# Optimization experiments

Hardware: AMD Instinct MI355X
Metric: run time of the kernel (lower is better)

## Reference

```python
import jax, jax.numpy as jnp
import numpy as np

EPS = 1e-5
H, W, C, NCLS = 8, 16, 64, 8

def _bn_params(key, c):
    k1, k2, k3, k4 = jax.random.split(key, 4)
    gamma = jax.random.uniform(k1, (c,), minval=0.5, maxval=1.5)
    beta = 0.1 * jax.random.normal(k2, (c,))
    mean = 0.1 * jax.random.normal(k3, (c,))
    var = jax.random.uniform(k4, (c,), minval=0.5, maxval=1.5)
    return jnp.stack([gamma, beta, mean, var]).astype(jnp.float32)  # (4, c)

def bn2d(x, p):
    # eval-mode BatchNorm2d; p: (4, C); x: (B, C, H, W)
    g, b, m, v = p[0], p[1], p[2], p[3]
    s = g * jax.lax.rsqrt(v + EPS)
    return x * s[None, :, None, None] + (b - m * s)[None, :, None, None]

def bn1d_scalar(x, p):
    # eval-mode BatchNorm1d with 1 channel; p: (4, 1); x: (B, 1, F)
    g, b, m, v = p[0], p[1], p[2], p[3]
    s = g * jax.lax.rsqrt(v + EPS)
    return x * s + (b - m * s)

def conv_same(x, w, b):
    y = jax.lax.conv_general_dilated(x, w, (1, 1), 'SAME',
                                     dimension_numbers=('NCHW', 'OIHW', 'NCHW'))
    return y + b[None, :, None, None]

def setup_inputs() -> dict:
    key = jax.random.key(0)
    ks = jax.random.split(key, 24)
    B = 8192
    d = {}
    d['x'] = jax.random.normal(ks[0], (B, 1, H, W), dtype=jnp.float32)
    d['bn0'] = _bn_params(ks[1], 1)
    d['conv1_w'] = 0.1 * jax.random.normal(ks[2], (C, 1, 3, 3), dtype=jnp.float32)
    d['conv1_b'] = jnp.zeros((C,), jnp.float32)
    d['bn1'] = _bn_params(ks[3], C)
    d['conv2_w'] = (0.1 / np.sqrt(C)) * jax.random.normal(ks[4], (C, C, 3, 3), dtype=jnp.float32)
    d['conv2_b'] = jnp.zeros((C,), jnp.float32)
    d['bn2'] = _bn_params(ks[5], C)
    # LocallyConnected2d, kernel_size=1 -> per-pixel (out_c, in_c) weights
    d['lc3_w'] = (1.0 / np.sqrt(C)) * jax.random.normal(ks[6], (C, C, H, W), dtype=jnp.float32)
    d['bn3'] = _bn_params(ks[7], C)
    d['lc4_w'] = (1.0 / np.sqrt(C)) * jax.random.normal(ks[8], (C, C, H, W), dtype=jnp.float32)
    d['bn4'] = _bn_params(ks[9], C)
    F5 = H * W * C
    d['fc5_w'] = (1.0 / np.sqrt(F5)) * jax.random.normal(ks[10], (512, F5), dtype=jnp.float32)
    d['fc5_b'] = jnp.zeros((512,), jnp.float32)
    d['bn5'] = _bn_params(ks[11], 1)
    d['fc6_w'] = (1.0 / np.sqrt(512)) * jax.random.normal(ks[12], (512, 512), dtype=jnp.float32)
    d['fc6_b'] = jnp.zeros((512,), jnp.float32)
    d['bn6'] = _bn_params(ks[13], 1)
    d['fc7_w'] = (1.0 / np.sqrt(512)) * jax.random.normal(ks[14], (128, 512), dtype=jnp.float32)
    d['fc7_b'] = jnp.zeros((128,), jnp.float32)
    d['bn7'] = _bn_params(ks[15], 1)
    d['fc8_w'] = (1.0 / np.sqrt(128)) * jax.random.normal(ks[16], (NCLS, 128), dtype=jnp.float32)
    d['fc8_b'] = jnp.zeros((NCLS,), jnp.float32)
    return d

def reference(x, bn0, conv1_w, conv1_b, bn1, conv2_w, conv2_b, bn2,
              lc3_w, bn3, lc4_w, bn4, fc5_w, fc5_b, bn5,
              fc6_w, fc6_b, bn6, fc7_w, fc7_b, bn7, fc8_w, fc8_b):
    B = x.shape[0]
    # squeeze -> view(B, 16, 8) -> transpose(1,2) -> add channel dim
    h = jnp.swapaxes(x.reshape(B, W, H), 1, 2)[:, None]  # (B,1,H,W)
    h = bn2d(h, bn0)
    h = jax.nn.relu(bn2d(conv_same(h, conv1_w, conv1_b), bn1))
    h = jax.nn.relu(bn2d(conv_same(h, conv2_w, conv2_b), bn2))
    # locally connected, k=1: per-pixel channel mixing
    h = jax.nn.relu(bn2d(jnp.einsum('bchw,ochw->bohw', h, lc3_w), bn3))
    h = jax.nn.relu(bn2d(jnp.einsum('bchw,ochw->bohw', h, lc4_w), bn4))
    h = h.reshape(B, 1, -1)  # (B, 1, C*H*W)
    h = h @ fc5_w.T + fc5_b
    h = jax.nn.relu(bn1d_scalar(h, bn5))
    h = jax.nn.relu(bn1d_scalar(h @ fc6_w.T + fc6_b, bn6))
    h = jax.nn.relu(bn1d_scalar(h @ fc7_w.T + fc7_b, bn7))
    h = h @ fc8_w.T + fc8_b
    return h.reshape(B, NCLS)
```

## Files before the change

### kernel.cpp

```cpp
#include <hip/hip_runtime.h>

typedef unsigned short bf16_t;
typedef __attribute__((ext_vector_type(8))) short bf16x8;
typedef __attribute__((ext_vector_type(8))) unsigned short u16x8;
typedef __attribute__((ext_vector_type(4))) float f32x4;

#if defined(__has_builtin)
#if __has_builtin(__builtin_amdgcn_global_load_lds)
#define HAS_GLL 1
#endif
#endif

__device__ __forceinline__ float b2f(bf16_t u) {
    return __uint_as_float(((unsigned int)u) << 16);
}
__device__ __forceinline__ bf16_t f2b(float f) {
    unsigned int x = __float_as_uint(f);
    unsigned int r = x + 0x7fffu + ((x >> 16) & 1u);
    return (bf16_t)(r >> 16);
}
__device__ __forceinline__ float ldf(const void* p, int i, int isf) {
    return isf ? ((const float*)p)[i] : b2f(((const bf16_t*)p)[i]);
}

__device__ __forceinline__ void stg16(const bf16_t* g, bf16_t* l) {
#ifdef HAS_GLL
    __builtin_amdgcn_global_load_lds(
        (const __attribute__((address_space(1))) unsigned int*)g,
        (__attribute__((address_space(3))) unsigned int*)l,
        16, 0, 0);
#else
    *(uint4*)l = *(const uint4*)g;
#endif
}

#define OFF_S0T0 0
#define OFF_W1   16
#define OFF_S1   592
#define OFF_H1   656
#define OFF_S2   720
#define OFF_H2   784
#define OFF_S3   848
#define OFF_H3   912
#define OFF_S4   976
#define OFF_H4   1040
#define OFF_SC5  1104
#define OFF_H5   1112
#define OFF_SC6  1624
#define OFF_H6   1632
#define OFF_SC7  2144
#define OFF_H7   2152
#define OFF_W8   2280
#define OFF_B8   3304
#define OFF_FLAG 4032

__global__ void detect_kernel(const void* xraw, float* prm)
{
    if (threadIdx.x == 0 && blockIdx.x == 0) {
        const unsigned int* w = (const unsigned int*)xraw;
        int good = 0;
        for (int i = 0; i < 64; i++) {
            float f = __uint_as_float(w[i] << 16);
            float a = fabsf(f);
            if (a >= 0.0009765625f && a <= 16.0f) good++;
        }
        prm[OFF_FLAG] = (good >= 32) ? 0.0f : 1.0f;
    }
}

__global__ __launch_bounds__(256) void cvtb_kernel(
    const void* __restrict__ src, bf16_t* __restrict__ dst, int n,
    const float* __restrict__ prm)
{
    const int isf = prm[OFF_FLAG] > 0.5f;
    int i = blockIdx.x * 256 + threadIdx.x;
    if (i < n) dst[i] = isf ? f2b(((const float*)src)[i]) : ((const bf16_t*)src)[i];
}

__global__ __launch_bounds__(256) void pw2_kernel(
    const void* __restrict__ src, bf16_t* __restrict__ dst,
    const float* __restrict__ prm)
{
    const int isf = prm[OFF_FLAG] > 0.5f;
    int i = blockIdx.x * 256 + threadIdx.x;
    if (i >= 36864) return;
    int oc = i / 576, r = i - oc * 576;
    int tap = r >> 6, ic = r & 63;
    dst[i] = f2b(ldf(src, oc * 576 + ic * 9 + tap, isf));
}

__global__ __launch_bounds__(256) void pw34_kernel(
    const void* __restrict__ src, bf16_t* __restrict__ dst,
    const float* __restrict__ prm)
{
    const int isf = prm[OFF_FLAG] > 0.5f;
    int i = blockIdx.x * 256 + threadIdx.x;
    if (i >= 524288) return;
    int p = i >> 12, r = i & 4095;
    int oc = r >> 6, ic = r & 63;
    dst[i] = f2b(ldf(src, oc * 8192 + ic * 128 + p, isf));
}

__global__ __launch_bounds__(256) void pw5_kernel(
    const void* __restrict__ src, bf16_t* __restrict__ dst,
    const float* __restrict__ prm)
{
    const int isf = prm[OFF_FLAG] > 0.5f;
    int i = blockIdx.x * 256 + threadIdx.x;
    if (i >= 4194304) return;
    int nr = i >> 13, r = i & 8191;
    int p = r >> 6, c = r & 63;
    dst[i] = f2b(ldf(src, nr * 8192 + c * 128 + p, isf));
}

__global__ __launch_bounds__(256) void fold_params_kernel(
    const void* bn0p, const void* w1, const void* b1, const void* bn1p,
    const void* b2c, const void* bn2p, const void* bn3p, const void* bn4p,
    const void* b5, const void* bn5p, const void* b6, const void* bn6p,
    const void* b7, const void* bn7p, const void* w8, const void* b8,
    float* prm)
{
    const int isf = prm[OFF_FLAG] > 0.5f;
    const int t = threadIdx.x;

    if (t == 0) {
        float g = ldf(bn0p, 0, isf), be = ldf(bn0p, 1, isf);
        float m = ldf(bn0p, 2, isf), v = ldf(bn0p, 3, isf);
        float s = g * rsqrtf(v + 1e-5f);
        prm[OFF_S0T0] = s; prm[OFF_S0T0 + 1] = be - m * s;
    }
    for (int i = t; i < 576; i += 256) prm[OFF_W1 + i] = ldf(w1, i, isf);

    if (t < 64) {
        {
            float g = ldf(bn1p, t, isf), be = ldf(bn1p, 64 + t, isf);
            float m = ldf(bn1p, 128 + t, isf), v = ldf(bn1p, 192 + t, isf);
            float s = g * rsqrtf(v + 1e-5f);
            prm[OFF_S1 + t] = s;
            prm[OFF_H1 + t] = s * ldf(b1, t, isf) + (be - m * s);
        }
        {
            float g = ldf(bn2p, t, isf), be = ldf(bn2p, 64 + t, isf);
            float m = ldf(bn2p, 128 + t, isf), v = ldf(bn2p, 192 + t, isf);
            float s = g * rsqrtf(v + 1e-5f);
            prm[OFF_S2 + t] = s;
            prm[OFF_H2 + t] = s * ldf(b2c, t, isf) + (be - m * s);
        }
        {
            float g = ldf(bn3p, t, isf), be = ldf(bn3p, 64 + t, isf);
            float m = ldf(bn3p, 128 + t, isf), v = ldf(bn3p, 192 + t, isf);
            float s = g * rsqrtf(v + 1e-5f);
            prm[OFF_S3 + t] = s;
            prm[OFF_H3 + t] = be - m * s;
        }
        {
            float g = ldf(bn4p, t, isf), be = ldf(bn4p, 64 + t, isf);
            float m = ldf(bn4p, 128 + t, isf), v = ldf(bn4p, 192 + t, isf);
            float s = g * rsqrtf(v + 1e-5f);
            prm[OFF_S4 + t] = s;
            prm[OFF_H4 + t] = be - m * s;
        }
    }
    {
        float g = ldf(bn5p, 0, isf), be = ldf(bn5p, 1, isf);
        float m = ldf(bn5p, 2, isf), v = ldf(bn5p, 3, isf);
        float s = g * rsqrtf(v + 1e-5f);
        if (t == 0) prm[OFF_SC5] = s;
        for (int i = t; i < 512; i += 256)
            prm[OFF_H5 + i] = s * ldf(b5, i, isf) + (be - m * s);
    }
    {
        float g = ldf(bn6p, 0, isf), be = ldf(bn6p, 1, isf);
        float m = ldf(bn6p, 2, isf), v = ldf(bn6p, 3, isf);
        float s = g * rsqrtf(v + 1e-5f);
        if (t == 0) prm[OFF_SC6] = s;
        for (int i = t; i < 512; i += 256)
            prm[OFF_H6 + i] = s * ldf(b6, i, isf) + (be - m * s);
    }
    {
        float g = ldf(bn7p, 0, isf), be = ldf(bn7p, 1, isf);
        float m = ldf(bn7p, 2, isf), v = ldf(bn7p, 3, isf);
        float s = g * rsqrtf(v + 1e-5f);
        if (t == 0) prm[OFF_SC7] = s;
        if (t < 128) prm[OFF_H7 + t] = s * ldf(b7, t, isf) + (be - m * s);
    }
    for (int i = t; i < 1024; i += 256) prm[OFF_W8 + i] = ldf(w8, i, isf);
    if (t < 8) prm[OFF_B8 + t] = ldf(b8, t, isf);
}

__global__ __launch_bounds__(256) void conv1_kernel(
    const void* __restrict__ x, const float* __restrict__ prm,
    bf16_t* __restrict__ c1, int Bc, int c0)
{
    __shared__ float xn[180];
    __shared__ float w1s[576];

    const int t = threadIdx.x;
    const int b0 = blockIdx.x * 4;
    const int isf = prm[OFF_FLAG] > 0.5f;
    const float s0 = prm[OFF_S0T0], t0 = prm[OFF_S0T0 + 1];

    for (int i = t; i < 576; i += 256) w1s[i] = prm[OFF_W1 + i];

    const int pg  = t & 31;
    const int oc0 = (t >> 5) * 8;

    float s1[8], h1[8];
    #pragma unroll
    for (int j = 0; j < 8; j++) {
        s1[j] = prm[OFF_S1 + oc0 + j];
        h1[j] = prm[OFF_H1 + oc0 + j];
    }

    for (int s = 0; s < 4; s++) {
        const int b = b0 + s;
        __syncthreads();
        if (t < 180) {
            int row = t / 18, col = t - row * 18;
            float v = 0.f;
            if (row >= 1 && row <= 8 && col >= 1 && col <= 16)
                v = s0 * ldf(x, (c0 + b) * 128 + (col - 1) * 8 + (row - 1), isf) + t0;
            xn[t] = v;
        }
        __syncthreads();

        #pragma unroll
        for (int m = 0; m < 4; m++) {
            int p = pg + 32 * m;
            int h = p >> 4, w = p & 15;
            float r[9];
            #pragma unroll
            for (int dh = 0; dh < 3; dh++)
                #pragma unroll
                for (int dw = 0; dw < 3; dw++)
                    r[dh * 3 + dw] = xn[(h + dh) * 18 + (w + dw)];
            u16x8 o;
            #pragma unroll
            for (int j = 0; j < 8; j++) {
                float acc = 0.f;
                #pragma unroll
                for (int k = 0; k < 9; k++) acc += r[k] * w1s[(oc0 + j) * 9 + k];
                o[j] = f2b(fmaxf(s1[j] * acc + h1[j], 0.f));
            }
            *(u16x8*)(c1 + (size_t)p * Bc * 64 + (size_t)b * 64 + oc0) = o;
        }
    }
}

__global__ __launch_bounds__(256) void fused_mfma_kernel(
    const bf16_t* __restrict__ c1, const bf16_t* __restrict__ w2p,
    const bf16_t* __restrict__ w3p, const bf16_t* __restrict__ w4p,
    const float* __restrict__ prm, bf16_t* __restrict__ bufA, int Bc)
{
    __shared__ bf16_t sm[20480];
    const int t    = threadIdx.x;
    const int lane = t & 63;
    const int wv   = t >> 6;
    const int m0   = blockIdx.x * 256;
    const int p    = blockIdx.y;
    const int h    = p >> 4, w = p & 15;

    const int fr = lane & 15;
    const int fg = lane >> 4;
    const int swz4 = (fr >> 1) & 3;
    const int orow = fg * 4;
    const int ocol = fr;

    const int rA = t >> 2;
    const int gS = (t & 3) ^ ((t >> 3) & 3);

    f32x4 acc[4][4];
    #pragma unroll
    for (int i = 0; i < 4; i++)
        #pragma unroll
        for (int j = 0; j < 4; j++)
            acc[i][j] = (f32x4){0.f, 0.f, 0.f, 0.f};

    {
        if (h > 0 && w > 0) {
            const bf16_t* ab = c1 + (size_t)((h - 1) * 16 + (w - 1)) * Bc * 64
                             + (size_t)m0 * 64;
            #pragma unroll
            for (int u = 0; u < 4; u++) {
                const int c = t + 256 * u;
                const int row = c >> 2;
                const int g = (c & 3) ^ ((c >> 3) & 3);
                stg16(ab + row * 64 + g * 8, sm + c * 8);
            }
            stg16(w2p + rA * 576 + gS * 8, sm + 16384 + t * 8);
        }
    }
    for (int s = 0; s < 18; s++) {
        const int cur = s & 1;
        __syncthreads();
        if (s + 1 < 18) {
            const int s1 = s + 1;
            const int tap = s1 >> 1;
            const int dh = tap / 3 - 1, dw = tap % 3 - 1;
            const int hh = h + dh, ww = w + dw;
            if (hh >= 0 && hh < 8 && ww >= 0 && ww < 16) {
                const int nb = cur ^ 1;
                const int ic0 = (s1 & 1) * 32;
                const bf16_t* ab = c1 + (size_t)(hh * 16 + ww) * Bc * 64
                                 + (size_t)m0 * 64 + ic0;
                #pragma unroll
                for (int u = 0; u < 4; u++) {
                    const int c = t + 256 * u;
                    const int row = c >> 2;
                    const int g = (c & 3) ^ ((c >> 3) & 3);
                    stg16(ab + row * 64 + g * 8, sm + nb * 8192 + c * 8);
                }
                stg16(w2p + rA * 576 + tap * 64 + ic0 + gS * 8,
                      sm + 16384 + nb * 2048 + t * 8);
            }
        }
        {
            const int tap = s >> 1;
            const int dh = tap / 3 - 1, dw = tap % 3 - 1;
            const int hh = h + dh, ww = w + dw;
            if (hh >= 0 && hh < 8 && ww >= 0 && ww < 16) {
                const bf16_t* Ab = sm + cur * 8192;
                const bf16_t* Bb = sm + 16384 + cur * 2048;
                bf16x8 af[4], bf[4];
                #pragma unroll
                for (int i = 0; i < 4; i++)
                    af[i] = *(const bf16x8*)(Ab + ((wv * 64 + i * 16 + fr) * 4 + (fg ^ swz4)) * 8);
                #pragma unroll
                for (int j = 0; j < 4; j++)
                    bf[j] = *(const bf16x8*)(Bb + ((j * 16 + fr) * 4 + (fg ^ swz4)) * 8);
                #pragma unroll
                for (int i = 0; i < 4; i++)
                    #pragma unroll
                    for (int j = 0; j < 4; j++)
                        acc[i][j] = __builtin_amdgcn_mfma_f32_16x16x32_bf16(
                            af[i], bf[j], acc[i][j], 0, 0, 0);
            }
        }
    }
    __syncthreads();

    #pragma unroll
    for (int j = 0; j < 4; j++) {
        const int oc = j * 16 + ocol;
        const float s = prm[OFF_S2 + oc], hh2 = prm[OFF_H2 + oc];
        #pragma unroll
        for (int i = 0; i < 4; i++) {
            const int rb = wv * 64 + i * 16 + orow;
            #pragma unroll
            for (int r = 0; r < 4; r++)
                sm[(rb + r) * 72 + oc] = f2b(fmaxf(s * acc[i][j][r] + hh2, 0.f));
        }
    }
    __syncthreads();

    #pragma unroll
    for (int i = 0; i < 4; i++)
        #pragma unroll
        for (int j = 0; j < 4; j++)
            acc[i][j] = (f32x4){0.f, 0.f, 0.f, 0.f};

    for (int ks = 0; ks < 2; ks++) {
        stg16(w3p + (size_t)p * 4096 + rA * 64 + ks * 32 + gS * 8, sm + 18432 + t * 8);
        __syncthreads();
        bf16x8 af[4], bf[4];
        #pragma unroll
        for (int i = 0; i < 4; i++)
            af[i] = *(const bf16x8*)(sm + (wv * 64 + i * 16 + fr) * 72 + ks * 32 + fg * 8);
        #pragma unroll
        for (int j = 0; j < 4; j++)
            bf[j] = *(const bf16x8*)(sm + 18432 + ((j * 16 + fr) * 4 + (fg ^ swz4)) * 8);
        #pragma unroll
        for (int i = 0; i < 4; i++)
            #pragma unroll
            for (int j = 0; j < 4; j++)
                acc[i][j] = __builtin_amdgcn_mfma_f32_16x16x32_bf16(
                    af[i], bf[j], acc[i][j], 0, 0, 0);
        __syncthreads();
    }

    #pragma unroll
    for (int j = 0; j < 4; j++) {
        const int oc = j * 16 + ocol;
        const float s = prm[OFF_S3 + oc], hh3 = prm[OFF_H3 + oc];
        #pragma unroll
        for (int i = 0; i < 4; i++) {
            const int rb = wv * 64 + i * 16 + orow;
            #pragma unroll
            for (int r = 0; r < 4; r++)
                sm[(rb + r) * 72 + oc] = f2b(fmaxf(s * acc[i][j][r] + hh3, 0.f));
        }
    }
    __syncthreads();

    #pragma unroll
    for (int i = 0; i < 4; i++)
        #pragma unroll
        for (int j = 0; j < 4; j++)
            acc[i][j] = (f32x4){0.f, 0.f, 0.f, 0.f};

    for (int ks = 0; ks < 2; ks++) {
        stg16(w4p + (size_t)p * 4096 + rA * 64 + ks * 32 + gS * 8, sm + 18432 + t * 8);
        __syncthreads();
        bf16x8 af[4], bf[4];
        #pragma unroll
        for (int i = 0; i < 4; i++)
            af[i] = *(const bf16x8*)(sm + (wv * 64 + i * 16 + fr) * 72 + ks * 32 + fg * 8);
        #pragma unroll
        for (int j = 0; j < 4; j++)
            bf[j] = *(const bf16x8*)(sm + 18432 + ((j * 16 + fr) * 4 + (fg ^ swz4)) * 8);
        #pragma unroll
        for (int i = 0; i < 4; i++)
            #pragma unroll
            for (int j = 0; j < 4; j++)
                acc[i][j] = __builtin_amdgcn_mfma_f32_16x16x32_bf16(
                    af[i], bf[j], acc[i][j], 0, 0, 0);
        __syncthreads();
    }

    #pragma unroll
    for (int j = 0; j < 4; j++) {
        const int oc = j * 16 + ocol;
        const float s = prm[OFF_S4 + oc], hh4 = prm[OFF_H4 + oc];
        #pragma unroll
        for (int i = 0; i < 4; i++) {
            const int rb = wv * 64 + i * 16 + orow;
            #pragma unroll
            for (int r = 0; r < 4; r++)
                sm[(rb + r) * 72 + oc] = f2b(fmaxf(s * acc[i][j][r] + hh4, 0.f));
        }
    }
    __syncthreads();

    const int wrow = t >> 3, wc0 = (t & 7) * 8;
    #pragma unroll
    for (int pass = 0; pass < 8; pass++) {
        const int row = wrow + pass * 32;
        *(uint4*)(bufA + (size_t)(m0 + row) * 8192 + p * 64 + wc0) =
            *(const uint4*)(sm + row * 72 + wc0);
    }
}

__global__ __launch_bounds__(256) void gemm_mfma(
    const bf16_t* __restrict__ A, const bf16_t* __restrict__ W,
    const float* __restrict__ prm, int sc_off, int sh_off,
    bf16_t* __restrict__ out, int K, int N)
{
    __shared__ bf16_t sm[24576];
    const int t    = threadIdx.x;
    const int lane = t & 63;
    const int wv   = t >> 6;
    const int wr   = wv >> 1, wc = wv & 1;
    const int m0   = blockIdx.x * 128, n0 = blockIdx.y * 64;

    const int fr = lane & 15;
    const int fg = lane >> 4;
    const int swz8 = fr & 7;

    const bf16_t* srcA[4]; bf16_t* dstA[4];
    #pragma unroll
    for (int u = 0; u < 4; u++) {
        const int c = t + 256 * u;
        const int row = c >> 3;
        const int g = (c & 7) ^ (row & 7);
        srcA[u] = A + (size_t)(m0 + row) * K + g * 8;
        dstA[u] = sm + c * 8;
    }
    const bf16_t* srcB[2]; bf16_t* dstB[2];
    #pragma unroll
    for (int u = 0; u < 2; u++) {
        const int c = t + 256 * u;
        const int row = c >> 3;
        const int g = (c & 7) ^ (row & 7);
        srcB[u] = W + (size_t)(n0 + row) * K + g * 8;
        dstB[u] = sm + 16384 + c * 8;
    }

    f32x4 acc[4][2];
    #pragma unroll
    for (int i = 0; i < 4; i++)
        #pragma unroll
        for (int j = 0; j < 2; j++)
            acc[i][j] = (f32x4){0.f, 0.f, 0.f, 0.f};

    const int KS = K >> 6;

    #pragma unroll
    for (int u = 0; u < 4; u++) stg16(srcA[u], dstA[u]);
    #pragma unroll
    for (int u = 0; u < 2; u++) stg16(srcB[u], dstB[u]);

    for (int ks = 0; ks < KS; ks++) {
        const int cur = ks & 1;
        __syncthreads();
        if (ks + 1 < KS) {
            const int nb = cur ^ 1;
            const int kk = (ks + 1) << 6;
            #pragma unroll
            for (int u = 0; u < 4; u++) stg16(srcA[u] + kk, dstA[u] + nb * 8192);
            #pragma unroll
            for (int u = 0; u < 2; u++) stg16(srcB[u] + kk, dstB[u] + nb * 4096);
        }
        const bf16_t* Ab = sm + cur * 8192;
        const bf16_t* Bb = sm + 16384 + cur * 4096;
        bf16x8 af[4][2], bf2[2][2];
        #pragma unroll
        for (int i = 0; i < 4; i++)
            #pragma unroll
            for (int hh = 0; hh < 2; hh++) {
                const int r = wr * 64 + i * 16 + fr;
                const int g = hh * 4 + fg;
                af[i][hh] = *(const bf16x8*)(Ab + (r * 8 + (g ^ swz8)) * 8);
            }
        #pragma unroll
        for (int j = 0; j < 2; j++)
            #pragma unroll
            for (int hh = 0; hh < 2; hh++) {
                const int r = wc * 32 + j * 16 + fr;
                const int g = hh * 4 + fg;
                bf2[j][hh] = *(const bf16x8*)(Bb + (r * 8 + (g ^ swz8)) * 8);
            }
        #pragma unroll
        for (int hh = 0; hh < 2; hh++)
            #pragma unroll
            for (int i = 0; i < 4; i++)
                #pragma unroll
                for (int j = 0; j < 2; j++)
                    acc[i][j] = __builtin_amdgcn_mfma_f32_16x16x32_bf16(
                        af[i][hh], bf2[j][hh], acc[i][j], 0, 0, 0);
    }

    const float s    = prm[sc_off];
    const int   orow = fg * 4;
    const int   ocol = fr;
    #pragma unroll
    for (int j = 0; j < 2; j++) {
        const int n  = n0 + wc * 32 + j * 16 + ocol;
        const float sh = prm[sh_off + n];
        #pragma unroll
        for (int i = 0; i < 4; i++) {
            const int mb = m0 + wr * 64 + i * 16 + orow;
            #pragma unroll
            for (int r = 0; r < 4; r++) {
                float v = fmaxf(s * acc[i][j][r] + sh, 0.f);
                out[(size_t)(mb + r) * N + n] = f2b(v);
            }
        }
    }
}

__global__ __launch_bounds__(256) void fc8_kernel(
    const bf16_t* __restrict__ h, const float* __restrict__ prm,
    void* __restrict__ out, int c0)
{
    __shared__ float wsm[8 * 129];
    const int t = threadIdx.x;
    for (int i = t; i < 1024; i += 256) {
        int n = i >> 7, k = i & 127;
        wsm[n * 129 + k] = prm[OFF_W8 + i];
    }
    __syncthreads();
    const int isf = prm[OFF_FLAG] > 0.5f;
    const int bl = t >> 3, n = t & 7;
    const int b = c0 + blockIdx.x * 32 + bl;
    const bf16_t* hb = h + (size_t)(blockIdx.x * 32 + bl) * 128;
    float acc = prm[OFF_B8 + n];
    for (int k = 0; k < 128; k++) acc += b2f(hb[k]) * wsm[n * 129 + k];
    if (isf) ((float*)out)[(size_t)b * 8 + n] = acc;
    else     ((bf16_t*)out)[(size_t)b * 8 + n] = f2b(acc);
}

extern "C" void kernel_launch(void* const* d_in, const int* in_sizes, int n_in,
                              void* d_out, int out_size, void* d_ws, size_t ws_size,
                              hipStream_t stream)
{
    const void* x    = d_in[0];
    const void* bn0p = d_in[1];
    const void* w1   = d_in[2];
    const void* b1   = d_in[3];
    const void* bn1p = d_in[4];
    const void* w2   = d_in[5];
    const void* b2c  = d_in[6];
    const void* bn2p = d_in[7];
    const void* w3   = d_in[8];
    const void* bn3p = d_in[9];
    const void* w4   = d_in[10];
    const void* bn4p = d_in[11];
    const void* w5   = d_in[12];
    const void* b5   = d_in[13];
    const void* bn5p = d_in[14];
    const void* w6   = d_in[15];
    const void* b6   = d_in[16];
    const void* bn6p = d_in[17];
    const void* w7   = d_in[18];
    const void* b7   = d_in[19];
    const void* bn7p = d_in[20];
    const void* w8   = d_in[21];
    const void* b8   = d_in[22];

    char* base = (char*)d_ws;
    float*  prm = (float*)(base + 0);
    bf16_t* w2p = (bf16_t*)(base + 16384);
    bf16_t* w3p = (bf16_t*)(base + 90112);
    bf16_t* w4p = (bf16_t*)(base + 1138688);
    bf16_t* w5p = (bf16_t*)(base + 2187264);
    bf16_t* w6b = (bf16_t*)(base + 10575872);
    bf16_t* w7b = (bf16_t*)(base + 11100160);
    char*   acts = base + 11231232;

    const int B = 8192;
    const size_t FIXED = 11231232ull;

    detect_kernel<<<1, 64, 0, stream>>>(x, prm);
    fold_params_kernel<<<1, 256, 0, stream>>>(
        bn0p, w1, b1, bn1p, b2c, bn2p, bn3p, bn4p,
        b5, bn5p, b6, bn6p, b7, bn7p, w8, b8, prm);

    pw2_kernel<<<(36864 + 255) / 256, 256, 0, stream>>>(w2, w2p, prm);
    pw34_kernel<<<(524288 + 255) / 256, 256, 0, stream>>>(w3, w3p, prm);
    pw34_kernel<<<(524288 + 255) / 256, 256, 0, stream>>>(w4, w4p, prm);
    pw5_kernel<<<(4194304 + 255) / 256, 256, 0, stream>>>(w5, w5p, prm);
    cvtb_kernel<<<(262144 + 255) / 256, 256, 0, stream>>>(w6, w6b, 262144, prm);
    cvtb_kernel<<<(65536 + 255) / 256, 256, 0, stream>>>(w7, w7b, 65536, prm);

    const int Bf = 4096;
    const size_t FULL_NEED = FIXED + (size_t)Bf * 16384ull + (size_t)B * 18688ull;

    if (ws_size >= FULL_NEED) {
        bf16_t* c1   = (bf16_t*)acts;
        bf16_t* bufA = c1 + (size_t)Bf * 8192;
        bf16_t* bufC = bufA + (size_t)B * 8192;
        bf16_t* bufD = bufC + (size_t)B * 512;
        bf16_t* bufE = bufD + (size_t)B * 512;

        for (int c0 = 0; c0 < B; c0 += Bf) {
            conv1_kernel<<<Bf / 4, 256, 0, stream>>>(x, prm, c1, Bf, c0);
            fused_mfma_kernel<<<dim3(Bf / 256, 128), 256, 0, stream>>>(
                c1, w2p, w3p, w4p, prm, bufA + (size_t)c0 * 8192, Bf);
        }
        gemm_mfma<<<dim3(B / 128, 8), 256, 0, stream>>>(
            bufA, w5p, prm, OFF_SC5, OFF_H5, bufC, 8192, 512);
        gemm_mfma<<<dim3(B / 128, 8), 256, 0, stream>>>(
            bufC, w6b, prm, OFF_SC6, OFF_H6, bufD, 512, 512);
        gemm_mfma<<<dim3(B / 128, 2), 256, 0, stream>>>(
            bufD, w7b, prm, OFF_SC7, OFF_H7, bufE, 512, 128);
        fc8_kernel<<<B / 32, 256, 0, stream>>>(bufE, prm, d_out, 0);
    } else {
        size_t avail = (ws_size > FIXED) ? (ws_size - FIXED) : 0;
        int Bc = 8192;
        while (Bc > 256 && (size_t)Bc * 35072ull > avail) Bc >>= 1;

        bf16_t* c1   = (bf16_t*)acts;
        bf16_t* bufA = c1 + (size_t)Bc * 8192;
        bf16_t* bufC = bufA + (size_t)Bc * 8192;
        bf16_t* bufD = bufC + (size_t)Bc * 512;
        bf16_t* bufE = bufD + (size_t)Bc * 512;

        for (int c0 = 0; c0 < B; c0 += Bc) {
            conv1_kernel<<<Bc / 4, 256, 0, stream>>>(x, prm, c1, Bc, c0);
            fused_mfma_kernel<<<dim3(Bc / 256, 128), 256, 0, stream>>>(
                c1, w2p, w3p, w4p, prm, bufA, Bc);
            gemm_mfma<<<dim3(Bc / 128, 8), 256, 0, stream>>>(
                bufA, w5p, prm, OFF_SC5, OFF_H5, bufC, 8192, 512);
            gemm_mfma<<<dim3(Bc / 128, 8), 256, 0, stream>>>(
                bufC, w6b, prm, OFF_SC6, OFF_H6, bufD, 512, 512);
            gemm_mfma<<<dim3(Bc / 128, 2), 256, 0, stream>>>(
                bufD, w7b, prm, OFF_SC7, OFF_H7, bufE, 512, 128);
            fc8_kernel<<<Bc / 32, 256, 0, stream>>>(bufE, prm, d_out, c0);
        }
    }
}
```

Measured before the change: 444.4 us.

## Merge weight-prep launches and prefetch LC weights into registers in fused kernel

Six weight permute/convert kernels are merged into one setup kernel covering all ranges, cutting five launches. In the fused conv2/LC kernel, the per-pixel LC3/LC4 weight tiles are loaded into registers at kernel start, so they no longer block on global loads between stages; they are written to shared memory from registers with fewer barriers. Address arithmetic for the conv2 staging loop is simplified and the tap loop is unrolled. The cost is extra live registers across the conv2 stage, which may reduce occupancy.

```diff
diff --git a/kernel.cpp b/kernel.cpp
--- a/kernel.cpp
+++ b/kernel.cpp
@@ -68,49 +68,43 @@
     }
 }
 
-__global__ __launch_bounds__(256) void cvtb_kernel(
-    const void* __restrict__ src, bf16_t* __restrict__ dst, int n,
+__global__ __launch_bounds__(256) void setup_kernel(
+    const void* __restrict__ w2, const void* __restrict__ w3,
+    const void* __restrict__ w4, const void* __restrict__ w5,
+    const void* __restrict__ w6, const void* __restrict__ w7,
+    bf16_t* __restrict__ w2p, bf16_t* __restrict__ w3p,
+    bf16_t* __restrict__ w4p, bf16_t* __restrict__ w5p,
+    bf16_t* __restrict__ w6b, bf16_t* __restrict__ w7b,
     const float* __restrict__ prm)
 {
     const int isf = prm[OFF_FLAG] > 0.5f;
-    int i = blockIdx.x * 256 + threadIdx.x;
-    if (i < n) dst[i] = isf ? f2b(((const float*)src)[i]) : ((const bf16_t*)src)[i];
-}
-
-__global__ __launch_bounds__(256) void pw2_kernel(
-    const void* __restrict__ src, bf16_t* __restrict__ dst,
-    const float* __restrict__ prm)
-{
-    const int isf = prm[OFF_FLAG] > 0.5f;
-    int i = blockIdx.x * 256 + threadIdx.x;
-    if (i >= 36864) return;
-    int oc = i / 576, r = i - oc * 576;
-    int tap = r >> 6, ic = r & 63;
-    dst[i] = f2b(ldf(src, oc * 576 + ic * 9 + tap, isf));
-}
-
-__global__ __launch_bounds__(256) void pw34_kernel(
-    const void* __restrict__ src, bf16_t* __restrict__ dst,
-    const float* __restrict__ prm)
-{
-    const int isf = prm[OFF_FLAG] > 0.5f;
-    int i = blockIdx.x * 256 + threadIdx.x;
-    if (i >= 524288) return;
-    int p = i >> 12, r = i & 4095;
-    int oc = r >> 6, ic = r & 63;
-    dst[i] = f2b(ldf(src, oc * 8192 + ic * 128 + p, isf));
-}
-
-__global__ __launch_bounds__(256) void pw5_kernel(
-    const void* __restrict__ src, bf16_t* __restrict__ dst,
-    const float* __restrict__ prm)
-{
-    const int isf = prm[OFF_FLAG] > 0.5f;
-    int i = blockIdx.x * 256 + threadIdx.x;
-    if (i >= 4194304) return;
-    int nr = i >> 13, r = i & 8191;
-    int p = r >> 6, c = r & 63;
-    dst[i] = f2b(ldf(src, nr * 8192 + c * 128 + p, isf));
+    const int i = blockIdx.x * 256 + threadIdx.x;
+    if (i < 36864) {
+        int oc = i / 576, r = i - oc * 576;
+        int tap = r >> 6, ic = r & 63;
+        w2p[i] = f2b(ldf(w2, oc * 576 + ic * 9 + tap, isf));
+    } else if (i < 561152) {
+        int j = i - 36864;
+        int p = j >> 12, r = j & 4095;
+        int oc = r >> 6, ic = r & 63;
+        w3p[j] = f2b(ldf(w3, oc * 8192 + ic * 128 + p, isf));
+    } else if (i < 1085440) {
+        int j = i - 561152;
+        int p = j >> 12, r = j & 4095;
+        int oc = r >> 6, ic = r & 63;
+        w4p[j] = f2b(ldf(w4, oc * 8192 + ic * 128 + p, isf));
+    } else if (i < 5279744) {
+        int j = i - 1085440;
+        int nr = j >> 13, r = j & 8191;
+        int p = r >> 6, c = r & 63;
+        w5p[j] = f2b(ldf(w5, nr * 8192 + c * 128 + p, isf));
+    } else if (i < 5541888) {
+        int j = i - 5279744;
+        w6b[j] = isf ? f2b(((const float*)w6)[j]) : ((const bf16_t*)w6)[j];
+    } else if (i < 5607424) {
+        int j = i - 5541888;
+        w7b[j] = isf ? f2b(((const float*)w7)[j]) : ((const bf16_t*)w7)[j];
+    }
 }
 
 __global__ __launch_bounds__(256) void fold_params_kernel(
@@ -266,8 +260,20 @@
     const int orow = fg * 4;
     const int ocol = fr;
 
-    const int rA = t >> 2;
-    const int gS = (t & 3) ^ ((t >> 3) & 3);
+    const int gS    = (t & 3) ^ ((t >> 3) & 3);
+    const int rA    = t >> 2;
+    const int coff0 = rA * 64 + gS * 8;
+    const int w2off = rA * 576 + gS * 8;
+
+    u16x8 wr3[2], wr4[2];
+    {
+        const bf16_t* w3b = w3p + (size_t)p * 4096 + coff0;
+        const bf16_t* w4b = w4p + (size_t)p * 4096 + coff0;
+        wr3[0] = *(const u16x8*)(w3b);
+        wr3[1] = *(const u16x8*)(w3b + 32);
+        wr4[0] = *(const u16x8*)(w4b);
+        wr4[1] = *(const u16x8*)(w4b + 32);
+    }
 
     f32x4 acc[4][4];
     #pragma unroll
@@ -276,42 +282,35 @@
         for (int j = 0; j < 4; j++)
             acc[i][j] = (f32x4){0.f, 0.f, 0.f, 0.f};
 
+    const bf16_t* c1b = c1 + (size_t)m0 * 64 + coff0;
+    const size_t planeStride = (size_t)Bc * 64;
+
     {
         if (h > 0 && w > 0) {
-            const bf16_t* ab = c1 + (size_t)((h - 1) * 16 + (w - 1)) * Bc * 64
-                             + (size_t)m0 * 64;
-            #pragma unroll
-            for (int u = 0; u < 4; u++) {
-                const int c = t + 256 * u;
-                const int row = c >> 2;
-                const int g = (c & 3) ^ ((c >> 3) & 3);
-                stg16(ab + row * 64 + g * 8, sm + c * 8);
-            }
-            stg16(w2p + rA * 576 + gS * 8, sm + 16384 + t * 8);
-        }
-    }
+            const bf16_t* ab = c1b + (size_t)((h - 1) * 16 + (w - 1)) * planeStride;
+            #pragma unroll
+            for (int u = 0; u < 4; u++)
+                stg16(ab + u * 4096, sm + t * 8 + u * 2048);
+            stg16(w2p + w2off, sm + 16384 + t * 8);
+        }
+    }
+    #pragma unroll
     for (int s = 0; s < 18; s++) {
         const int cur = s & 1;
         __syncthreads();
         if (s + 1 < 18) {
-            const int s1 = s + 1;
+            const int s1  = s + 1;
             const int tap = s1 >> 1;
             const int dh = tap / 3 - 1, dw = tap % 3 - 1;
             const int hh = h + dh, ww = w + dw;
             if (hh >= 0 && hh < 8 && ww >= 0 && ww < 16) {
-                const int nb = cur ^ 1;
+                const int nb  = cur ^ 1;
                 const int ic0 = (s1 & 1) * 32;
-                const bf16_t* ab = c1 + (size_t)(hh * 16 + ww) * Bc * 64
-                                 + (size_t)m0 * 64 + ic0;
+                const bf16_t* ab = c1b + (size_t)(hh * 16 + ww) * planeStride + ic0;
                 #pragma unroll
-                for (int u = 0; u < 4; u++) {
-                    const int c = t + 256 * u;
-                    const int row = c >> 2;
-                    const int g = (c & 3) ^ ((c >> 3) & 3);
-                    stg16(ab + row * 64 + g * 8, sm + nb * 8192 + c * 8);
-                }
-                stg16(w2p + rA * 576 + tap * 64 + ic0 + gS * 8,
-                      sm + 16384 + nb * 2048 + t * 8);
+                for (int u = 0; u < 4; u++)
+                    stg16(ab + u * 4096, sm + nb * 8192 + t * 8 + u * 2048);
+                stg16(w2p + w2off + tap * 64 + ic0, sm + 16384 + nb * 2048 + t * 8);
             }
         }
         {
@@ -351,6 +350,7 @@
                 sm[(rb + r) * 72 + oc] = f2b(fmaxf(s * acc[i][j][r] + hh2, 0.f));
         }
     }
+    *(u16x8*)(sm + 18432 + t * 8) = wr3[0];
     __syncthreads();
 
     #pragma unroll
@@ -359,9 +359,13 @@
         for (int j = 0; j < 4; j++)
             acc[i][j] = (f32x4){0.f, 0.f, 0.f, 0.f};
 
+    #pragma unroll
     for (int ks = 0; ks < 2; ks++) {
-        stg16(w3p + (size_t)p * 4096 + rA * 64 + ks * 32 + gS * 8, sm + 18432 + t * 8);
-        __syncthreads();
+        if (ks == 1) {
+            __syncthreads();
+            *(u16x8*)(sm + 18432 + t * 8) = wr3[1];
+            __syncthreads();
+        }
         bf16x8 af[4], bf[4];
         #pragma unroll
         for (int i = 0; i < 4; i++)
@@ -375,7 +379,6 @@
             for (int j = 0; j < 4; j++)
                 acc[i][j] = __builtin_amdgcn_mfma_f32_16x16x32_bf16(
                     af[i], bf[j], acc[i][j], 0, 0, 0);
-        __syncthreads();
     }
 
     #pragma unroll
@@ -391,6 +394,8 @@
         }
     }
     __syncthreads();
+    *(u16x8*)(sm + 18432 + t * 8) = wr4[0];
+    __syncthreads();
 
     #pragma unroll
     for (int i = 0; i < 4; i++)
@@ -398,9 +403,13 @@
         for (int j = 0; j < 4; j++)
             acc[i][j] = (f32x4){0.f, 0.f, 0.f, 0.f};
 
+    #pragma unroll
     for (int ks = 0; ks < 2; ks++) {
-        stg16(w4p + (size_t)p * 4096 + rA * 64 + ks * 32 + gS * 8, sm + 18432 + t * 8);
-        __syncthreads();
+        if (ks == 1) {
+            __syncthreads();
+            *(u16x8*)(sm + 18432 + t * 8) = wr4[1];
+            __syncthreads();
+        }
         bf16x8 af[4], bf[4];
         #pragma unroll
         for (int i = 0; i < 4; i++)
@@ -414,7 +423,6 @@
             for (int j = 0; j < 4; j++)
                 acc[i][j] = __builtin_amdgcn_mfma_f32_16x16x32_bf16(
                     af[i], bf[j], acc[i][j], 0, 0, 0);
-        __syncthreads();
     }
 
     #pragma unroll
@@ -614,13 +622,8 @@
     fold_params_kernel<<<1, 256, 0, stream>>>(
         bn0p, w1, b1, bn1p, b2c, bn2p, bn3p, bn4p,
         b5, bn5p, b6, bn6p, b7, bn7p, w8, b8, prm);
-
-    pw2_kernel<<<(36864 + 255) / 256, 256, 0, stream>>>(w2, w2p, prm);
-    pw34_kernel<<<(524288 + 255) / 256, 256, 0, stream>>>(w3, w3p, prm);
-    pw34_kernel<<<(524288 + 255) / 256, 256, 0, stream>>>(w4, w4p, prm);
-    pw5_kernel<<<(4194304 + 255) / 256, 256, 0, stream>>>(w5, w5p, prm);
-    cvtb_kernel<<<(262144 + 255) / 256, 256, 0, stream>>>(w6, w6b, 262144, prm);
-    cvtb_kernel<<<(65536 + 255) / 256, 256, 0, stream>>>(w7, w7b, 65536, prm);
+    setup_kernel<<<21904, 256, 0, stream>>>(
+        w2, w3, w4, w5, w6, w7, w2p, w3p, w4p, w5p, w6b, w7b, prm);
 
     const int Bf = 4096;
     const size_t FULL_NEED = FIXED + (size_t)Bf * 16384ull + (size_t)B * 18688ull;
```

After: 436.8 us. Within noise of the previous version (-1.7%).
